# Kernel tuning notes

Hardware: AMD Instinct MI355X
Metric: run time of the kernel (lower is better)

Reference implementation:

```python
import jax, jax.numpy as jnp
import numpy as np
import math

D_MODEL = 512
N_HEADS = 8
D_K = D_MODEL // N_HEADS
D_FF = 2048
EPS = 1e-6


def _layer_norm(x, gamma, beta):
    # Matches the torch module: unbiased std (ddof=1), divide by (std + eps)
    mean = jnp.mean(x, axis=-1, keepdims=True)
    std = jnp.std(x, axis=-1, ddof=1, keepdims=True)
    return gamma * (x - mean) / (std + EPS) + beta


def setup_inputs() -> dict:
    key = jax.random.key(0)
    ks = jax.random.split(key, 16)
    B, S = 4, 2048
    s_attn = 1.0 / math.sqrt(D_MODEL)
    s_ff1 = 1.0 / math.sqrt(D_MODEL)
    s_ff2 = 1.0 / math.sqrt(D_FF)
    inp = {
        "x": jax.random.normal(ks[0], (B, S, D_MODEL), dtype=jnp.float32),
        "mask": jnp.ones((1, 1, S, S), dtype=jnp.int32),
        "wq": jax.random.normal(ks[1], (D_MODEL, D_MODEL), jnp.float32) * s_attn,
        "bq": jnp.zeros((D_MODEL,), jnp.float32),
        "wk": jax.random.normal(ks[2], (D_MODEL, D_MODEL), jnp.float32) * s_attn,
        "bk": jnp.zeros((D_MODEL,), jnp.float32),
        "wv": jax.random.normal(ks[3], (D_MODEL, D_MODEL), jnp.float32) * s_attn,
        "bv": jnp.zeros((D_MODEL,), jnp.float32),
        "wo": jax.random.normal(ks[4], (D_MODEL, D_MODEL), jnp.float32) * s_attn,
        "bo": jnp.zeros((D_MODEL,), jnp.float32),
        "w1": jax.random.normal(ks[5], (D_MODEL, D_FF), jnp.float32) * s_ff1,
        "b1": jnp.zeros((D_FF,), jnp.float32),
        "w2": jax.random.normal(ks[6], (D_FF, D_MODEL), jnp.float32) * s_ff2,
        "b2": jnp.zeros((D_MODEL,), jnp.float32),
        "g1": jnp.ones((1, 1, D_MODEL), jnp.float32),
        "be1": jnp.zeros((1, 1, D_MODEL), jnp.float32),
        "g2": jnp.ones((1, 1, D_MODEL), jnp.float32),
        "be2": jnp.zeros((1, 1, D_MODEL), jnp.float32),
    }
    return inp


def reference(x, mask, wq, bq, wk, bk, wv, bv, wo, bo, w1, b1, w2, b2, g1, be1, g2, be2):
    B, S, _ = x.shape
    # --- residual 1: pre-norm self-attention ---
    xn = _layer_norm(x, g1, be1)
    q = (xn @ wq + bq).reshape(B, S, N_HEADS, D_K).transpose(0, 2, 1, 3)
    k = (xn @ wk + bk).reshape(B, S, N_HEADS, D_K).transpose(0, 2, 1, 3)
    v = (xn @ wv + bv).reshape(B, S, N_HEADS, D_K).transpose(0, 2, 1, 3)
    # NOTE: source uses floor division `//` by sqrt(d_k) (a faithful-ly kept bug)
    scores = jnp.floor_divide(jnp.einsum("bhqd,bhkd->bhqk", q, k), math.sqrt(D_K))
    scores = jnp.where(mask == 0, jnp.float32(-1e9), scores)
    attn = jax.nn.softmax(scores, axis=-1)
    ctx = jnp.einsum("bhqk,bhkd->bhqd", attn, v)
    ctx = ctx.transpose(0, 2, 1, 3).reshape(B, S, D_MODEL)
    x = x + (ctx @ wo + bo)
    # --- residual 2: pre-norm feed-forward ---
    xn2 = _layer_norm(x, g2, be2)
    ff = jax.nn.relu(xn2 @ w1 + b1) @ w2 + b2
    return x + ff
```

## Files before the change

### kernel.cpp

```cpp
#include <hip/hip_runtime.h>
#include <cmath>

#define SEQ 2048
#define DM 512
#define DFF 2048
#define NH 8
#define DKH 64
#define NROWS 8192

typedef __attribute__((ext_vector_type(8))) short bf16x8;
typedef __attribute__((ext_vector_type(16))) float f32x16;

__device__ __forceinline__ ushort f2bf(float f) {
    uint u = __float_as_uint(f);
    u += 0x7fff + ((u >> 16) & 1);
    return (ushort)(u >> 16);
}
__device__ __forceinline__ float bf2f(ushort h) {
    return __uint_as_float(((uint)h) << 16);
}
__device__ __forceinline__ uint cvtpk_bf16(float a, float b) {
    uint r;
    asm("v_cvt_pk_bf16_f32 %0, %1, %2" : "=v"(r) : "v"(a), "v"(b));
    return r;
}
__device__ __forceinline__ void gl_lds16(const void* g, void* l) {
    __builtin_amdgcn_global_load_lds(
        (const __attribute__((address_space(1))) void*)g,
        (__attribute__((address_space(3))) void*)l, 16, 0, 0);
}
__device__ __forceinline__ void* swz(char* base, int row, int col) {
    int byte = (row << 7) + (col << 1);
    byte ^= (row & 7) << 4;
    return base + byte;
}
__device__ __forceinline__ void* swzg(char* base, int row, int k) {
    int byte = (row << 7) + (k << 1);
    byte ^= ((row >> 2) & 7) << 4;
    return base + byte;
}
__device__ __forceinline__ void* swzv(char* base, int row, int col) {
    int byte = (row << 8) + (col << 1);
    byte ^= (row & 7) << 4;
    return base + byte;
}

template<bool SPLIT>
__device__ __forceinline__ void ln_row(const float* __restrict__ x,
        const float* __restrict__ g, const float* __restrict__ b,
        ushort* __restrict__ oh, ushort* __restrict__ ol, int row, int t) {
    const float* xr = x + (size_t)row * DM + t * 8;
    float v[8];
    *(float4*)&v[0] = *(const float4*)(xr);
    *(float4*)&v[4] = *(const float4*)(xr + 4);
    float s = 0.f;
    #pragma unroll
    for (int j = 0; j < 8; ++j) s += v[j];
    #pragma unroll
    for (int m = 32; m > 0; m >>= 1) s += __shfl_xor(s, m);
    float mean = s * (1.0f / DM);
    float ss = 0.f;
    #pragma unroll
    for (int j = 0; j < 8; ++j) { float d = v[j] - mean; ss += d * d; }
    #pragma unroll
    for (int m = 32; m > 0; m >>= 1) ss += __shfl_xor(ss, m);
    float inv = 1.0f / (sqrtf(ss * (1.0f / (DM - 1))) + 1e-6f);
    float gv[8], bv[8];
    *(float4*)&gv[0] = *(const float4*)(g + t * 8);
    *(float4*)&gv[4] = *(const float4*)(g + t * 8 + 4);
    *(float4*)&bv[0] = *(const float4*)(b + t * 8);
    *(float4*)&bv[4] = *(const float4*)(b + t * 8 + 4);
    union { ushort us[8]; float4 f4; } ph, pl;
    #pragma unroll
    for (int j = 0; j < 8; ++j) {
        float o = gv[j] * (v[j] - mean) * inv + bv[j];
        ushort hb = f2bf(o);
        ph.us[j] = hb;
        if (SPLIT) pl.us[j] = f2bf(o - bf2f(hb));
    }
    *(float4*)(oh + (size_t)row * DM + t * 8) = ph.f4;
    if (SPLIT) *(float4*)(ol + (size_t)row * DM + t * 8) = pl.f4;
}

template<bool SPLIT>
__global__ __launch_bounds__(256) void ln_kernel(const float* __restrict__ x,
        const float* __restrict__ g, const float* __restrict__ b,
        ushort* __restrict__ oh, ushort* __restrict__ ol) {
    ln_row<SPLIT>(x, g, b, oh, ol, blockIdx.x * 4 + (threadIdx.x >> 6),
                  threadIdx.x & 63);
}

__global__ __launch_bounds__(256) void prep(
        const float* __restrict__ wq, const float* __restrict__ wk,
        const float* __restrict__ wv, const float* __restrict__ wo,
        const float* __restrict__ w1, const float* __restrict__ w2,
        const int* __restrict__ mask, const float* __restrict__ x,
        const float* __restrict__ g1, const float* __restrict__ be1,
        ushort* __restrict__ qh, ushort* __restrict__ ql,
        ushort* __restrict__ kh, ushort* __restrict__ vh,
        ushort* __restrict__ oh,
        ushort* __restrict__ w1t, ushort* __restrict__ w2t,
        ushort* __restrict__ mb, unsigned char* __restrict__ mflag,
        ushort* __restrict__ xn_h, ushort* __restrict__ xn_l) {
    __shared__ float tile[64][65];
    int id = blockIdx.x;
    int t = threadIdx.x;
    if (id < 768) {
        const float* W;
        ushort* Th;
        ushort* Tl = nullptr;
        int K, N, k0, n0;
        bool split = false;
        if (id < 256) {
            int z = id >> 6, r = id & 63;
            W = (z == 0) ? wq : (z == 1) ? wk : (z == 2) ? wv : wo;
            Th = (z == 0) ? qh : (z == 1) ? kh : (z == 2) ? vh : oh;
            Tl = (z == 0) ? ql : nullptr;
            split = (z == 0);
            K = DM; N = DM;
            k0 = (r >> 3) * 64; n0 = (r & 7) * 64;
        } else if (id < 512) {
            int r = id - 256;
            W = w1; Th = w1t; K = DM; N = DFF;
            k0 = (r & 7) * 64; n0 = (r >> 3) * 64;
        } else {
            int r = id - 512;
            W = w2; Th = w2t; K = DFF; N = DM;
            k0 = (r & 31) * 64; n0 = (r >> 5) * 64;
        }
        {
            int kr = t >> 2, c0 = (t & 3) * 16;
            const float* src = W + (size_t)(k0 + kr) * N + n0 + c0;
            #pragma unroll
            for (int j = 0; j < 4; ++j)
                *(float4*)&tile[kr][c0 + j * 4] = *(const float4*)(src + j * 4);
        }
        __syncthreads();
        int n = t >> 2, kc = (t & 3) * 16;
        union { ushort us[16]; float4 f4[2]; } ph, pl;
        #pragma unroll
        for (int j = 0; j < 16; ++j) {
            float v = tile[kc + j][n];
            ushort hb = f2bf(v);
            ph.us[j] = hb;
            pl.us[j] = f2bf(v - bf2f(hb));
        }
        ushort* dh = Th + (size_t)(n0 + n) * K + k0 + kc;
        *(float4*)(dh) = ph.f4[0];
        *(float4*)(dh + 8) = ph.f4[1];
        if (split) {
            ushort* dl = Tl + (size_t)(n0 + n) * K + k0 + kc;
            *(float4*)(dl) = pl.f4[0];
            *(float4*)(dl + 8) = pl.f4[1];
        }
    } else if (id < 1280) {
        int row = (id - 768) * 4 + (t >> 6);
        int lane = t & 63;
        ushort neg = f2bf(-1e9f);
        unsigned long long bal[4];
        #pragma unroll
        for (int u = 0; u < 4; ++u) {
            int base = row * SEQ + u * 512 + lane * 8;
            int4 a = *(const int4*)(mask + base);
            int4 c = *(const int4*)(mask + base + 4);
            union { ushort us[8]; float4 f4; } o;
            o.us[0] = a.x ? (ushort)0 : neg;
            o.us[1] = a.y ? (ushort)0 : neg;
            o.us[2] = a.z ? (ushort)0 : neg;
            o.us[3] = a.w ? (ushort)0 : neg;
            o.us[4] = c.x ? (ushort)0 : neg;
            o.us[5] = c.y ? (ushort)0 : neg;
            o.us[6] = c.z ? (ushort)0 : neg;
            o.us[7] = c.w ? (ushort)0 : neg;
            *(float4*)(mb + base) = o.f4;
            bool ok = a.x && a.y && a.z && a.w && c.x && c.y && c.z && c.w;
            bal[u] = __ballot(ok);
        }
        if (lane < 32) {
            int u = lane >> 3;
            unsigned long long bsel = bal[0];
            bsel = (u == 1) ? bal[1] : bsel;
            bsel = (u == 2) ? bal[2] : bsel;
            bsel = (u == 3) ? bal[3] : bsel;
            int byte = (int)((bsel >> ((lane & 7) * 8)) & 0xFFull);
            mflag[row * 32 + lane] = (byte == 0xFF) ? 1 : 0;
        }
    } else {
        ln_row<true>(x, g1, be1, xn_h, xn_l,
                     (id - 1280) * 4 + (t >> 6), t & 63);
    }
}

template<bool RELU, bool HASRES, int OUT>
__global__ __launch_bounds__(256) void mgemm(
        const ushort* __restrict__ Ah, const ushort* __restrict__ Bth,
        const float* __restrict__ bias, const float* __restrict__ resid,
        float* __restrict__ Cf, ushort* __restrict__ Cbh,
        int M, int N, int K) {
    __shared__ __align__(16) char smem[65536];
    int tid = threadIdx.x;
    int lane = tid & 63, w = tid >> 6;
    int ln31 = lane & 31, hi = lane >> 5;
    int mh = (w >> 1) * 64, nh = (w & 1) * 64;
    int gx = gridDim.x;
    int nwg = gx * gridDim.y;
    int flat = blockIdx.y * gx + blockIdx.x;
    int sid = (flat & 7) * (nwg >> 3) + (flat >> 3);
    int n0 = (sid % gx) * 128;
    int m0 = (sid / gx) * 128;

    f32x16 acc[2][2];
    #pragma unroll
    for (int i = 0; i < 2; ++i)
        #pragma unroll
        for (int j = 0; j < 2; ++j)
            #pragma unroll
            for (int r = 0; r < 16; ++r) acc[i][j][r] = 0.f;

    auto stage = [&](char* Abuf, char* Bbuf, int k0) {
        #pragma unroll
        for (int c = 0; c < 4; ++c) {
            int ch = w * 4 + c;
            int r = ch * 8 + (lane >> 3);
            int u = (lane & 7) ^ ((r >> 2) & 7);
            gl_lds16(Ah + (size_t)(m0 + r) * K + k0 + u * 8, Abuf + ch * 1024);
            gl_lds16(Bth + (size_t)(n0 + r) * K + k0 + u * 8, Bbuf + ch * 1024);
        }
    };

    char* A0 = smem;
    char* B0 = smem + 16384;
    char* A1 = smem + 32768;
    char* B1 = smem + 49152;

    stage(A0, B0, 0);
    __syncthreads();
    int nk = K / 64;
    for (int kt = 0; kt < nk; ++kt) {
        char* Ac = (kt & 1) ? A1 : A0;
        char* Bc = (kt & 1) ? B1 : B0;
        if (kt + 1 < nk)
            stage((kt & 1) ? A0 : A1, (kt & 1) ? B0 : B1, (kt + 1) * 64);
        __builtin_amdgcn_s_setprio(1);
        #pragma unroll
        for (int km = 0; km < 4; ++km) {
            int kk = km * 16 + hi * 8;
            bf16x8 ah[2], bh[2];
            ah[0] = *(bf16x8*)swzg(Ac, mh + ln31, kk);
            ah[1] = *(bf16x8*)swzg(Ac, mh + 32 + ln31, kk);
            bh[0] = *(bf16x8*)swzg(Bc, nh + ln31, kk);
            bh[1] = *(bf16x8*)swzg(Bc, nh + 32 + ln31, kk);
            #pragma unroll
            for (int mi = 0; mi < 2; ++mi)
                #pragma unroll
                for (int ni = 0; ni < 2; ++ni)
                    acc[mi][ni] = __builtin_amdgcn_mfma_f32_32x32x16_bf16(
                        ah[mi], bh[ni], acc[mi][ni], 0, 0, 0);
        }
        __builtin_amdgcn_s_setprio(0);
        __syncthreads();
    }
    float bv[2];
    bv[0] = bias[n0 + nh + ln31];
    bv[1] = bias[n0 + nh + 32 + ln31];
    #pragma unroll
    for (int mi = 0; mi < 2; ++mi)
        #pragma unroll
        for (int ni = 0; ni < 2; ++ni) {
            int n = n0 + nh + ni * 32 + ln31;
            #pragma unroll
            for (int r = 0; r < 16; ++r) {
                int m = m0 + mh + mi * 32 + (r & 3) + 8 * (r >> 2) + 4 * hi;
                float v = acc[mi][ni][r] + bv[ni];
                if (HASRES) v += resid[(size_t)m * N + n];
                if (RELU) v = fmaxf(v, 0.f);
                size_t idx = (size_t)m * N + n;
                if (OUT == 0) Cf[idx] = v;
                else Cbh[idx] = f2bf(v);
            }
        }
}

template<bool RELU, bool HASRES, int OUT, bool COMB>
__global__ __launch_bounds__(256) void mgemm64(
        const ushort* __restrict__ Ah, const ushort* __restrict__ Bth,
        const float* __restrict__ bias, const float* __restrict__ resid,
        float* __restrict__ Cf, ushort* __restrict__ Cbh,
        const ushort* __restrict__ p0, const ushort* __restrict__ p1,
        const float2* __restrict__ mlp, int M, int N, int K) {
    __shared__ __align__(16) char smem[32768];
    int tid = threadIdx.x;
    int lane = tid & 63, w = tid >> 6;
    int ln31 = lane & 31, hi = lane >> 5;
    int mh = (w >> 1) * 32, nh = (w & 1) * 32;
    int gx = gridDim.x;
    int nwg = gx * gridDim.y;
    int flat = blockIdx.y * gx + blockIdx.x;
    int sid = (flat & 7) * (nwg >> 3) + (flat >> 3);
    int n0 = (sid % gx) * 64;
    int m0 = (sid / gx) * 64;

    f32x16 acc;
    #pragma unroll
    for (int r = 0; r < 16; ++r) acc[r] = 0.f;

    auto stage = [&](char* Abuf, char* Bbuf, int k0) {
        #pragma unroll
        for (int c = 0; c < 2; ++c) {
            int ch = w * 2 + c;
            int r = ch * 8 + (lane >> 3);
            int u = (lane & 7) ^ ((r >> 2) & 7);
            if (COMB) {
                int m = m0 + r;
                int b = m >> 11, q = m & (SEQ - 1);
                int bh = b * 8 + (k0 >> 6);
                size_t pbase = ((size_t)bh * SEQ + q) * DKH + u * 8;
                union { ushort us[8]; float4 f4; } a0, a1, o;
                a0.f4 = *(const float4*)(p0 + pbase);
                a1.f4 = *(const float4*)(p1 + pbase);
                float2 e0 = mlp[(size_t)bh * SEQ + q];
                float2 e1 = mlp[((size_t)32 + bh) * SEQ + q];
                float mm = fmaxf(e0.x, e1.x);
                float w0 = __expf(e0.x - mm), w1 = __expf(e1.x - mm);
                float inv = 1.0f / (e0.y * w0 + e1.y * w1);
                #pragma unroll
                for (int j = 0; j < 8; ++j)
                    o.us[j] = f2bf((bf2f(a0.us[j]) * w0 + bf2f(a1.us[j]) * w1) * inv);
                *(float4*)(Abuf + ch * 1024 + lane * 16) = o.f4;
            } else {
                gl_lds16(Ah + (size_t)(m0 + r) * K + k0 + u * 8, Abuf + ch * 1024);
            }
            gl_lds16(Bth + (size_t)(n0 + r) * K + k0 + u * 8, Bbuf + ch * 1024);
        }
    };

    char* A0 = smem;
    char* B0 = smem + 8192;
    char* A1 = smem + 16384;
    char* B1 = smem + 24576;

    stage(A0, B0, 0);
    __syncthreads();
    int nk = K / 64;
    for (int kt = 0; kt < nk; ++kt) {
        char* Ac = (kt & 1) ? A1 : A0;
        char* Bc = (kt & 1) ? B1 : B0;
        if (kt + 1 < nk)
            stage((kt & 1) ? A0 : A1, (kt & 1) ? B0 : B1, (kt + 1) * 64);
        __builtin_amdgcn_s_setprio(1);
        #pragma unroll
        for (int km = 0; km < 4; ++km) {
            int kk = km * 16 + hi * 8;
            bf16x8 a = *(bf16x8*)swzg(Ac, mh + ln31, kk);
            bf16x8 b = *(bf16x8*)swzg(Bc, nh + ln31, kk);
            acc = __builtin_amdgcn_mfma_f32_32x32x16_bf16(a, b, acc, 0, 0, 0);
        }
        __builtin_amdgcn_s_setprio(0);
        __syncthreads();
    }
    float bv = bias[n0 + nh + ln31];
    int n = n0 + nh + ln31;
    #pragma unroll
    for (int r = 0; r < 16; ++r) {
        int m = m0 + mh + (r & 3) + 8 * (r >> 2) + 4 * hi;
        float v = acc[r] + bv;
        if (HASRES) v += resid[(size_t)m * N + n];
        if (RELU) v = fmaxf(v, 0.f);
        size_t idx = (size_t)m * N + n;
        if (OUT == 0) Cf[idx] = v;
        else Cbh[idx] = f2bf(v);
    }
}

__global__ __launch_bounds__(256) void qkv_gemm(
        const ushort* __restrict__ Ah, const ushort* __restrict__ Al,
        const ushort* __restrict__ Bth, const ushort* __restrict__ Btl,
        const float* __restrict__ bq, const float* __restrict__ bk,
        const float* __restrict__ bv_, ushort* __restrict__ q_h,
        ushort* __restrict__ k_h, ushort* __restrict__ v_t) {
    const int K = DM, N = DM;
    __shared__ __align__(16) char smem[65536];
    char* As_h = smem;
    char* Bs_h = smem + 16384;
    char* As_l = smem + 32768;
    char* Bs_l = smem + 49152;
    int tid = threadIdx.x;
    int lane = tid & 63, w = tid >> 6;
    int ln31 = lane & 31, hi = lane >> 5;
    int mh = (w >> 1) * 64, nh = (w & 1) * 64;
    int gx = gridDim.x;
    int nwg = gx * gridDim.y;
    int flat = blockIdx.y * gx + blockIdx.x;
    int sid = (flat & 7) * (nwg >> 3) + (flat >> 3);
    int n0 = (sid % gx) * 128;
    int m0 = (sid / gx) * 128;
    bool issplit = (n0 < 512);

    f32x16 acc[2][2];
    #pragma unroll
    for (int i = 0; i < 2; ++i)
        #pragma unroll
        for (int j = 0; j < 2; ++j)
            #pragma unroll
            for (int r = 0; r < 16; ++r) acc[i][j][r] = 0.f;

    for (int k0 = 0; k0 < K; k0 += 64) {
        #pragma unroll
        for (int c = 0; c < 4; ++c) {
            int ch = w * 4 + c;
            int r = ch * 8 + (lane >> 3);
            int u = (lane & 7) ^ ((r >> 2) & 7);
            gl_lds16(Ah + (size_t)(m0 + r) * K + k0 + u * 8, As_h + ch * 1024);
            gl_lds16(Bth + (size_t)(n0 + r) * K + k0 + u * 8, Bs_h + ch * 1024);
            if (issplit) {
                gl_lds16(Al + (size_t)(m0 + r) * K + k0 + u * 8, As_l + ch * 1024);
                gl_lds16(Btl + (size_t)(n0 + r) * K + k0 + u * 8, Bs_l + ch * 1024);
            }
        }
        __syncthreads();
        __builtin_amdgcn_s_setprio(1);
        #pragma unroll
        for (int km = 0; km < 4; ++km) {
            int kk = km * 16 + hi * 8;
            bf16x8 ah[2], bh[2];
            ah[0] = *(bf16x8*)swzg(As_h, mh + ln31, kk);
            ah[1] = *(bf16x8*)swzg(As_h, mh + 32 + ln31, kk);
            bh[0] = *(bf16x8*)swzg(Bs_h, nh + ln31, kk);
            bh[1] = *(bf16x8*)swzg(Bs_h, nh + 32 + ln31, kk);
            if (issplit) {
                bf16x8 al[2], bl[2];
                al[0] = *(bf16x8*)swzg(As_l, mh + ln31, kk);
                al[1] = *(bf16x8*)swzg(As_l, mh + 32 + ln31, kk);
                bl[0] = *(bf16x8*)swzg(Bs_l, nh + ln31, kk);
                bl[1] = *(bf16x8*)swzg(Bs_l, nh + 32 + ln31, kk);
                #pragma unroll
                for (int mi = 0; mi < 2; ++mi)
                    #pragma unroll
                    for (int ni = 0; ni < 2; ++ni) {
                        acc[mi][ni] = __builtin_amdgcn_mfma_f32_32x32x16_bf16(
                            ah[mi], bh[ni], acc[mi][ni], 0, 0, 0);
                        acc[mi][ni] = __builtin_amdgcn_mfma_f32_32x32x16_bf16(
                            ah[mi], bl[ni], acc[mi][ni], 0, 0, 0);
                        acc[mi][ni] = __builtin_amdgcn_mfma_f32_32x32x16_bf16(
                            al[mi], bh[ni], acc[mi][ni], 0, 0, 0);
                    }
            } else {
                #pragma unroll
                for (int mi = 0; mi < 2; ++mi)
                    #pragma unroll
                    for (int ni = 0; ni < 2; ++ni)
                        acc[mi][ni] = __builtin_amdgcn_mfma_f32_32x32x16_bf16(
                            ah[mi], bh[ni], acc[mi][ni], 0, 0, 0);
            }
        }
        __builtin_amdgcn_s_setprio(0);
        __syncthreads();
    }
    if (n0 < 512) {
        float bvv[2];
        bvv[0] = bq[n0 + nh + ln31];
        bvv[1] = bq[n0 + nh + 32 + ln31];
        #pragma unroll
        for (int mi = 0; mi < 2; ++mi)
            #pragma unroll
            for (int ni = 0; ni < 2; ++ni) {
                int n = n0 + nh + ni * 32 + ln31;
                #pragma unroll
                for (int r = 0; r < 16; ++r) {
                    int m = m0 + mh + mi * 32 + (r & 3) + 8 * (r >> 2) + 4 * hi;
                    float v = (acc[mi][ni][r] + bvv[ni]) * 0.125f;
                    q_h[(size_t)m * N + n] = f2bf(v);
                }
            }
    } else if (n0 < 1024) {
        int ncol0 = n0 - 512;
        float bvv[2];
        bvv[0] = bk[ncol0 + nh + ln31];
        bvv[1] = bk[ncol0 + nh + 32 + ln31];
        #pragma unroll
        for (int mi = 0; mi < 2; ++mi)
            #pragma unroll
            for (int ni = 0; ni < 2; ++ni) {
                int n = ncol0 + nh + ni * 32 + ln31;
                #pragma unroll
                for (int r = 0; r < 16; ++r) {
                    int m = m0 + mh + mi * 32 + (r & 3) + 8 * (r >> 2) + 4 * hi;
                    k_h[(size_t)m * N + n] = f2bf(acc[mi][ni][r] + bvv[ni]);
                }
            }
    } else {
        int ncol0 = n0 & 511;
        float bvv[2];
        bvv[0] = bv_[ncol0 + nh + ln31];
        bvv[1] = bv_[ncol0 + nh + 32 + ln31];
        __syncthreads();
        #pragma unroll
        for (int mi = 0; mi < 2; ++mi)
            #pragma unroll
            for (int ni = 0; ni < 2; ++ni) {
                int nloc = nh + ni * 32 + ln31;
                #pragma unroll
                for (int r = 0; r < 16; ++r) {
                    int mloc = mh + mi * 32 + (r & 3) + 8 * (r >> 2) + 4 * hi;
                    *(ushort*)swzv(smem, mloc, nloc) =
                        f2bf(acc[mi][ni][r] + bvv[ni]);
                }
            }
        __syncthreads();
        int nloc = tid >> 1, half = tid & 1;
        int nglob = ncol0 + nloc;
        int h = nglob >> 6, d = nglob & 63;
        int b = m0 >> 11;
        int s0 = (m0 & (SEQ - 1)) + half * 64;
        ushort* dst = v_t + (((size_t)(b * 8 + h) * DKH + d) * SEQ) + s0;
        #pragma unroll
        for (int gblk = 0; gblk < 8; ++gblk) {
            union { ushort us[8]; float4 f4; } ov;
            #pragma unroll
            for (int j = 0; j < 8; ++j)
                ov.us[j] = *(ushort*)swzv(smem, half * 64 + gblk * 8 + j, nloc);
            *(float4*)(dst + gblk * 8) = ov.f4;
        }
    }
}

__global__ __launch_bounds__(512) void attn_kernel(
        const ushort* __restrict__ Qh, const ushort* __restrict__ Khg,
        const ushort* __restrict__ Vtg, const ushort* __restrict__ mb,
        const unsigned char* __restrict__ mflag,
        ushort* __restrict__ pctx0, ushort* __restrict__ pctx1,
        float2* __restrict__ ml) {
    __shared__ __align__(16) char smem[32768];
    int tid = threadIdx.x;
    int w = tid >> 6, lane = tid & 63;
    int ln31 = lane & 31, hi = lane >> 5;
    bool hib = (hi != 0);
    int f = blockIdx.y * gridDim.x + blockIdx.x;
    int g = (f & 7) * 64 + (f >> 3);
    int bh = g >> 4, rest = g & 15;
    int part = rest >> 3, qb = rest & 7;
    int b = bh >> 3, h = bh & 7;
    int q0 = qb * 256;
    size_t brow = (size_t)b * SEQ;
    int hcol = h * DKH;
    int ktbeg = part * 16, ktend = ktbeg + 16;

    auto stage_kv = [&](char* buf, int kt) {
        #pragma unroll
        for (int c = 0; c < 2; ++c) {
            int q = w * 2 + c;
            int r = (q & 7) * 8 + (lane >> 3);
            int u = (lane & 7) ^ (r & 7);
            const ushort* src = (q < 8)
                ? Khg + (brow + kt * 64 + r) * DM + hcol + u * 8
                : Vtg + ((size_t)bh * DKH + r) * SEQ + kt * 64 + u * 8;
            gl_lds16(src, buf + q * 1024);
        }
    };

    {
        #pragma unroll
        for (int c = 0; c < 4; ++c) {
            int ch = w * 4 + c;
            int r = ch * 8 + (lane >> 3);
            int u = (lane & 7) ^ (r & 7);
            gl_lds16(Qh + (brow + q0 + r) * DM + hcol + u * 8,
                     smem + ch * 1024);
        }
    }
    __syncthreads();
    bf16x8 qfh[4];
    {
        int qr = w * 32 + ln31;
        #pragma unroll
        for (int c = 0; c < 4; ++c)
            qfh[c] = *(bf16x8*)swz(smem, qr, c * 16 + hi * 8);
    }
    __syncthreads();
    stage_kv(smem + (ktbeg & 1) * 16384, ktbeg);
    __syncthreads();

    f32x16 ctx0, ctx1;
    #pragma unroll
    for (int r = 0; r < 16; ++r) { ctx0[r] = 0.f; ctx1[r] = 0.f; }
    float m_i = -1e30f, l_i = 0.f;
    int qglob = q0 + w * 32 + ln31;
    const ushort* mrow = mb + (size_t)qglob * SEQ;

    for (int kt = ktbeg; kt < ktend; ++kt) {
        char* cur = smem + (kt & 1) * 16384;
        if (kt + 1 < ktend)
            stage_kv(smem + ((kt + 1) & 1) * 16384, kt + 1);
        unsigned char fl = mflag[qglob * 32 + kt];
        bool domask = !__all(fl != 0);
        ushort4 mpre[8];
        if (domask) {
            #pragma unroll
            for (int i = 0; i < 8; ++i)
                mpre[i] = *(const ushort4*)(mrow + kt * 64 + i * 8 + hi * 4);
        }
        char* KhL = cur;
        char* VtL = cur + 8192;
        #pragma unroll
        for (int ksub = 0; ksub < 2; ++ksub) {
            f32x16 s;
            #pragma unroll
            for (int r = 0; r < 16; ++r) s[r] = 0.f;
            __builtin_amdgcn_s_setprio(1);
            #pragma unroll
            for (int c = 0; c < 4; ++c) {
                bf16x8 ka = *(bf16x8*)swz(KhL, ksub * 32 + ln31, c * 16 + hi * 8);
                s = __builtin_amdgcn_mfma_f32_32x32x16_bf16(ka, qfh[c], s, 0, 0, 0);
            }
            __builtin_amdgcn_s_setprio(0);
            if (domask) {
                #pragma unroll
                for (int rg = 0; rg < 4; ++rg) {
                    ushort4 mv = mpre[ksub * 4 + rg];
                    ushort mu[4] = {mv.x, mv.y, mv.z, mv.w};
                    #pragma unroll
                    for (int j = 0; j < 4; ++j) {
                        int r = rg * 4 + j;
                        s[r] = floorf(s[r]) + bf2f(mu[j]);
                    }
                }
            } else {
                #pragma unroll
                for (int r = 0; r < 16; ++r) s[r] = floorf(s[r]);
            }
            float t0 = fmaxf(fmaxf(s[0], s[1]), fmaxf(s[2], s[3]));
            float t1 = fmaxf(fmaxf(s[4], s[5]), fmaxf(s[6], s[7]));
            float t2 = fmaxf(fmaxf(s[8], s[9]), fmaxf(s[10], s[11]));
            float t3 = fmaxf(fmaxf(s[12], s[13]), fmaxf(s[14], s[15]));
            float tmax = fmaxf(fmaxf(t0, t1), fmaxf(t2, t3));
            tmax = fmaxf(tmax, __shfl_xor(tmax, 32));
            if (!__all(tmax <= m_i)) {
                float newm = fmaxf(m_i, tmax);
                float scl = __expf(m_i - newm);
                m_i = newm;
                l_i *= scl;
                #pragma unroll
                for (int r = 0; r < 16; ++r) { ctx0[r] *= scl; ctx1[r] *= scl; }
            }
            #pragma unroll
            for (int r = 0; r < 16; ++r) s[r] = __expf(s[r] - m_i);
            {
                float p0 = (s[0] + s[4]) + (s[8] + s[12]);
                float p1 = (s[1] + s[5]) + (s[9] + s[13]);
                float p2 = (s[2] + s[6]) + (s[10] + s[14]);
                float p3 = (s[3] + s[7]) + (s[11] + s[15]);
                float psum = (p0 + p1) + (p2 + p3);
                psum += __shfl_xor(psum, 32);
                l_i += psum;
            }
            uint pk0[4], pk1[4];
            #pragma unroll
            for (int rg = 0; rg < 4; ++rg) {
                pk0[rg] = cvtpk_bf16(s[rg * 4 + 0], s[rg * 4 + 1]);
                pk1[rg] = cvtpk_bf16(s[rg * 4 + 2], s[rg * 4 + 3]);
            }
            bf16x8 pb[2];
            #pragma unroll
            for (int cc = 0; cc < 2; ++cc) {
                uint A0 = pk0[cc * 2], A1 = pk1[cc * 2];
                uint B0 = pk0[cc * 2 + 1], B1 = pk1[cc * 2 + 1];
                uint send0 = hib ? A0 : B0;
                uint send1 = hib ? A1 : B1;
                uint own0  = hib ? B0 : A0;
                uint own1  = hib ? B1 : A1;
                uint recv0 = (uint)__shfl_xor((int)send0, 32);
                uint recv1 = (uint)__shfl_xor((int)send1, 32);
                union { uint u[4]; bf16x8 v; } pbu;
                pbu.u[0] = hib ? recv0 : own0;
                pbu.u[1] = hib ? recv1 : own1;
                pbu.u[2] = hib ? own0 : recv0;
                pbu.u[3] = hib ? own1 : recv1;
                pb[cc] = pbu.v;
            }
            __builtin_amdgcn_s_setprio(1);
            #pragma unroll
            for (int cc = 0; cc < 2; ++cc) {
                int c = ksub * 2 + cc;
                bf16x8 va0 = *(bf16x8*)swz(VtL, ln31, c * 16 + hi * 8);
                bf16x8 va1 = *(bf16x8*)swz(VtL, 32 + ln31, c * 16 + hi * 8);
                ctx0 = __builtin_amdgcn_mfma_f32_32x32x16_bf16(va0, pb[cc], ctx0, 0, 0, 0);
                ctx1 = __builtin_amdgcn_mfma_f32_32x32x16_bf16(va1, pb[cc], ctx1, 0, 0, 0);
            }
            __builtin_amdgcn_s_setprio(0);
        }
        __syncthreads();
    }

    ushort* P = part ? pctx1 : pctx0;
    size_t pbase = ((size_t)bh * SEQ + qglob) * DKH;
    #pragma unroll
    for (int r = 0; r < 16; ++r) {
        int d = (r & 3) + 8 * (r >> 2) + 4 * hi;
        P[pbase + d] = f2bf(ctx0[r]);
        P[pbase + 32 + d] = f2bf(ctx1[r]);
    }
    if (hi == 0)
        ml[((size_t)part * 32 + bh) * SEQ + qglob] = make_float2(m_i, l_i);
}

extern "C" void kernel_launch(void* const* d_in, const int* in_sizes, int n_in,
                              void* d_out, int out_size, void* d_ws, size_t ws_size,
                              hipStream_t stream) {
    const float* x    = (const float*)d_in[0];
    const int*   mask = (const int*)d_in[1];
    const float* wq = (const float*)d_in[2];
    const float* bq = (const float*)d_in[3];
    const float* wk = (const float*)d_in[4];
    const float* bk = (const float*)d_in[5];
    const float* wv = (const float*)d_in[6];
    const float* bv = (const float*)d_in[7];
    const float* wo = (const float*)d_in[8];
    const float* bo = (const float*)d_in[9];
    const float* w1 = (const float*)d_in[10];
    const float* b1 = (const float*)d_in[11];
    const float* w2 = (const float*)d_in[12];
    const float* b2 = (const float*)d_in[13];
    const float* g1  = (const float*)d_in[14];
    const float* be1 = (const float*)d_in[15];
    const float* g2  = (const float*)d_in[16];
    const float* be2 = (const float*)d_in[17];
    float* out = (float*)d_out;

    char* ws = (char*)d_ws;
    const size_t MiB = 1024 * 1024;
    ushort* xn_h = (ushort*)(ws);
    ushort* xn_l = (ushort*)(ws + 8 * MiB);
    ushort* q_h  = (ushort*)(ws + 16 * MiB);
    ushort* k_h  = (ushort*)(ws + 32 * MiB);
    ushort* v_t  = (ushort*)(ws + 56 * MiB);
    ushort* wqkvt_h = (ushort*)(ws + 64 * MiB);
    ushort* wqt_l   = (ushort*)(ws + 66 * MiB);
    ushort* wot_h = (ushort*)(ws + 67 * MiB);
    unsigned char* mflag = (unsigned char*)(ws + 67 * MiB + 512 * 1024);
    ushort* w1t_h = (ushort*)(ws + 68 * MiB);
    ushort* w2t_h = (ushort*)(ws + 70 * MiB);
    ushort* mb    = (ushort*)(ws + 72 * MiB);
    ushort* pctx0 = (ushort*)(ws + 80 * MiB);
    ushort* pctx1 = (ushort*)(ws + 88 * MiB);
    float2* ml    = (float2*)(ws + 96 * MiB);
    ushort* xn2  = xn_l;
    ushort* ff1  = q_h;

    dim3 blk256(256);
    prep<<<3328, blk256, 0, stream>>>(
        wq, wk, wv, wo, w1, w2, mask, x, g1, be1,
        wqkvt_h, wqt_l, wqkvt_h + 512 * 512,
        wqkvt_h + 1024 * 512, wot_h, w1t_h, w2t_h, mb, mflag, xn_h, xn_l);
    qkv_gemm<<<dim3(12, NROWS / 128), blk256, 0, stream>>>(
        xn_h, xn_l, wqkvt_h, wqt_l, bq, bk, bv, q_h, k_h, v_t);
    {
        dim3 grid(32, 16);
        attn_kernel<<<grid, dim3(512), 0, stream>>>(
            q_h, k_h, v_t, mb, mflag, pctx0, pctx1, ml);
    }
    {
        dim3 grid(DM / 64, NROWS / 64);
        mgemm64<false,true,0,true><<<grid, blk256, 0, stream>>>(
            nullptr, wot_h, bo, x, out, nullptr, pctx0, pctx1, ml,
            NROWS, DM, DM);
    }
    ln_kernel<false><<<NROWS / 4, blk256, 0, stream>>>(out, g2, be2, xn2, nullptr);
    {
        dim3 grid(DFF / 128, NROWS / 128);
        mgemm<true,false,1><<<grid, blk256, 0, stream>>>(
            xn2, w1t_h, b1, nullptr, nullptr, ff1, NROWS, DFF, DM);
    }
    {
        dim3 grid(DM / 64, NROWS / 64);
        mgemm64<false,true,0,false><<<grid, blk256, 0, stream>>>(
            ff1, w2t_h, b2, out, out, nullptr, nullptr, nullptr, nullptr,
            NROWS, DM, DFF);
    }
}
```

Baseline: 217.0 us.

## Split attention KV range into four partitions and merge in output GEMM

After: 231.2 us. 6.6% more time.

```diff
diff --git a/kernel.cpp b/kernel.cpp
--- a/kernel.cpp
+++ b/kernel.cpp
@@ -287,6 +287,7 @@
         const float* __restrict__ bias, const float* __restrict__ resid,
         float* __restrict__ Cf, ushort* __restrict__ Cbh,
         const ushort* __restrict__ p0, const ushort* __restrict__ p1,
+        const ushort* __restrict__ p2, const ushort* __restrict__ p3,
         const float2* __restrict__ mlp, int M, int N, int K) {
     __shared__ __align__(16) char smem[32768];
     int tid = threadIdx.x;
@@ -315,17 +316,24 @@
                 int b = m >> 11, q = m & (SEQ - 1);
                 int bh = b * 8 + (k0 >> 6);
                 size_t pbase = ((size_t)bh * SEQ + q) * DKH + u * 8;
-                union { ushort us[8]; float4 f4; } a0, a1, o;
+                union { ushort us[8]; float4 f4; } a0, a1, a2, a3, o;
                 a0.f4 = *(const float4*)(p0 + pbase);
                 a1.f4 = *(const float4*)(p1 + pbase);
-                float2 e0 = mlp[(size_t)bh * SEQ + q];
-                float2 e1 = mlp[((size_t)32 + bh) * SEQ + q];
-                float mm = fmaxf(e0.x, e1.x);
+                a2.f4 = *(const float4*)(p2 + pbase);
+                a3.f4 = *(const float4*)(p3 + pbase);
+                size_t mlb = (size_t)bh * SEQ + q;
+                float2 e0 = mlp[mlb];
+                float2 e1 = mlp[mlb + (size_t)32 * SEQ];
+                float2 e2 = mlp[mlb + (size_t)64 * SEQ];
+                float2 e3 = mlp[mlb + (size_t)96 * SEQ];
+                float mm = fmaxf(fmaxf(e0.x, e1.x), fmaxf(e2.x, e3.x));
                 float w0 = __expf(e0.x - mm), w1 = __expf(e1.x - mm);
-                float inv = 1.0f / (e0.y * w0 + e1.y * w1);
+                float w2 = __expf(e2.x - mm), w3 = __expf(e3.x - mm);
+                float inv = 1.0f / (e0.y * w0 + e1.y * w1 + e2.y * w2 + e3.y * w3);
                 #pragma unroll
                 for (int j = 0; j < 8; ++j)
-                    o.us[j] = f2bf((bf2f(a0.us[j]) * w0 + bf2f(a1.us[j]) * w1) * inv);
+                    o.us[j] = f2bf((bf2f(a0.us[j]) * w0 + bf2f(a1.us[j]) * w1 +
+                                    bf2f(a2.us[j]) * w2 + bf2f(a3.us[j]) * w3) * inv);
                 *(float4*)(Abuf + ch * 1024 + lane * 16) = o.f4;
             } else {
                 gl_lds16(Ah + (size_t)(m0 + r) * K + k0 + u * 8, Abuf + ch * 1024);
@@ -528,7 +536,8 @@
         const ushort* __restrict__ Qh, const ushort* __restrict__ Khg,
         const ushort* __restrict__ Vtg, const ushort* __restrict__ mb,
         const unsigned char* __restrict__ mflag,
-        ushort* __restrict__ pctx0, ushort* __restrict__ pctx1,
+        ushort* __restrict__ p0, ushort* __restrict__ p1,
+        ushort* __restrict__ p2, ushort* __restrict__ p3,
         float2* __restrict__ ml) {
     __shared__ __align__(16) char smem[32768];
     int tid = threadIdx.x;
@@ -536,14 +545,14 @@
     int ln31 = lane & 31, hi = lane >> 5;
     bool hib = (hi != 0);
     int f = blockIdx.y * gridDim.x + blockIdx.x;
-    int g = (f & 7) * 64 + (f >> 3);
-    int bh = g >> 4, rest = g & 15;
+    int g = (f & 7) * 128 + (f >> 3);
+    int bh = g >> 5, rest = g & 31;
     int part = rest >> 3, qb = rest & 7;
     int b = bh >> 3, h = bh & 7;
     int q0 = qb * 256;
     size_t brow = (size_t)b * SEQ;
     int hcol = h * DKH;
-    int ktbeg = part * 16, ktend = ktbeg + 16;
+    int ktbeg = part * 8, ktend = ktbeg + 8;
 
     auto stage_kv = [&](char* buf, int kt) {
         #pragma unroll
@@ -645,11 +654,11 @@
             #pragma unroll
             for (int r = 0; r < 16; ++r) s[r] = __expf(s[r] - m_i);
             {
-                float p0 = (s[0] + s[4]) + (s[8] + s[12]);
-                float p1 = (s[1] + s[5]) + (s[9] + s[13]);
-                float p2 = (s[2] + s[6]) + (s[10] + s[14]);
-                float p3 = (s[3] + s[7]) + (s[11] + s[15]);
-                float psum = (p0 + p1) + (p2 + p3);
+                float p0s = (s[0] + s[4]) + (s[8] + s[12]);
+                float p1s = (s[1] + s[5]) + (s[9] + s[13]);
+                float p2s = (s[2] + s[6]) + (s[10] + s[14]);
+                float p3s = (s[3] + s[7]) + (s[11] + s[15]);
+                float psum = (p0s + p1s) + (p2s + p3s);
                 psum += __shfl_xor(psum, 32);
                 l_i += psum;
             }
@@ -691,7 +700,7 @@
         __syncthreads();
     }
 
-    ushort* P = part ? pctx1 : pctx0;
+    ushort* P = (part == 0) ? p0 : (part == 1) ? p1 : (part == 2) ? p2 : p3;
     size_t pbase = ((size_t)bh * SEQ + qglob) * DKH;
     #pragma unroll
     for (int r = 0; r < 16; ++r) {
@@ -742,6 +751,8 @@
     ushort* mb    = (ushort*)(ws + 72 * MiB);
     ushort* pctx0 = (ushort*)(ws + 80 * MiB);
     ushort* pctx1 = (ushort*)(ws + 88 * MiB);
+    ushort* pctx2 = (ushort*)(ws + 40 * MiB);
+    ushort* pctx3 = (ushort*)(ws + 48 * MiB);
     float2* ml    = (float2*)(ws + 96 * MiB);
     ushort* xn2  = xn_l;
     ushort* ff1  = q_h;
@@ -754,15 +765,15 @@
     qkv_gemm<<<dim3(12, NROWS / 128), blk256, 0, stream>>>(
         xn_h, xn_l, wqkvt_h, wqt_l, bq, bk, bv, q_h, k_h, v_t);
     {
-        dim3 grid(32, 16);
+        dim3 grid(32, 32);
         attn_kernel<<<grid, dim3(512), 0, stream>>>(
-            q_h, k_h, v_t, mb, mflag, pctx0, pctx1, ml);
+            q_h, k_h, v_t, mb, mflag, pctx0, pctx1, pctx2, pctx3, ml);
     }
     {
         dim3 grid(DM / 64, NROWS / 64);
         mgemm64<false,true,0,true><<<grid, blk256, 0, stream>>>(
-            nullptr, wot_h, bo, x, out, nullptr, pctx0, pctx1, ml,
-            NROWS, DM, DM);
+            nullptr, wot_h, bo, x, out, nullptr, pctx0, pctx1, pctx2, pctx3,
+            ml, NROWS, DM, DM);
     }
     ln_kernel<false><<<NROWS / 4, blk256, 0, stream>>>(out, g2, be2, xn2, nullptr);
     {
@@ -774,6 +785,6 @@
         dim3 grid(DM / 64, NROWS / 64);
         mgemm64<false,true,0,false><<<grid, blk256, 0, stream>>>(
             ff1, w2t_h, b2, out, out, nullptr, nullptr, nullptr, nullptr,
-            NROWS, DM, DFF);
-    }
-}
+            nullptr, nullptr, NROWS, DM, DFF);
+    }
+}
```
